# Optimization experiments

Hardware: AMD Instinct MI355X
Metric: run time of the kernel (lower is better)

The kernel has to match this reference:

```python
import jax, jax.numpy as jnp
import numpy as np

B, S, D, H = 4, 2048, 1024, 16
DK = D // H  # 64
THETA = 10000.0


def _rope(x, pos):
    # x: [..., s, d], pos: [s] int. Rotation-matrix RoPE applied to consecutive pairs.
    d = x.shape[-1]
    inv_freq = 1.0 / (THETA ** (jnp.arange(0, d, 2, dtype=jnp.float32) / d))  # [d/2]
    freqs = pos.astype(jnp.float32)[:, None] * inv_freq[None, :]             # [s, d/2]
    cos, sin = jnp.cos(freqs), jnp.sin(freqs)
    xr = x.reshape(x.shape[:-1] + (d // 2, 2))
    x0, x1 = xr[..., 0], xr[..., 1]
    y0 = cos * x0 - sin * x1
    y1 = sin * x0 + cos * x1
    return jnp.stack([y0, y1], axis=-1).reshape(x.shape)


def setup_inputs() -> dict:
    key = jax.random.key(0)
    ks = jax.random.split(key, 5)
    std = float(np.sqrt(2.0 / (D + D)))
    return {
        "x": jax.random.normal(ks[0], (B, S, D), dtype=jnp.float32),
        "token_positions": jnp.arange(S, dtype=jnp.int32),
        "wq": jax.random.normal(ks[1], (D, D), dtype=jnp.float32) * std,
        "wk": jax.random.normal(ks[2], (D, D), dtype=jnp.float32) * std,
        "wv": jax.random.normal(ks[3], (D, D), dtype=jnp.float32) * std,
        "wo": jax.random.normal(ks[4], (D, D), dtype=jnp.float32) * std,
    }


def reference(x, token_positions, wq, wk, wv, wo):
    # Linear layers use weight [out, in]: y = x @ W^T
    q = jnp.einsum('bsd,od->bso', x, wq).reshape(B, S, H, DK).transpose(0, 2, 1, 3)  # [b,h,s,dk]
    k = jnp.einsum('bsd,od->bso', x, wk).reshape(B, S, H, DK).transpose(0, 2, 1, 3)
    v = jnp.einsum('bsd,od->bso', x, wv).reshape(B, S, H, DK).transpose(0, 2, 1, 3)
    q = _rope(q, token_positions)
    k = _rope(k, token_positions)
    scores = jnp.einsum('bhqd,bhkd->bhqk', q, k) / jnp.sqrt(jnp.float32(DK))
    causal = jnp.tril(jnp.ones((S, S), dtype=bool))
    scores = jnp.where(causal, scores, jnp.finfo(scores.dtype).min)
    attn = jax.nn.softmax(scores, axis=-1)
    o = jnp.einsum('bhqk,bhkd->bhqd', attn, v)          # [b,h,s,dk]
    o = o.transpose(0, 2, 1, 3).reshape(B, S, D)        # [b,s,h*dk]
    return jnp.einsum('bsd,od->bso', o, wo)
```

## Files before the change

### kernel.cpp

```cpp
#include <hip/hip_runtime.h>
#include <hip/hip_bf16.h>
#include <stdint.h>

#define S_LEN 2048
#define NHEAD 16
#define BATCH 4

typedef __attribute__((ext_vector_type(8))) short short8;
typedef __attribute__((ext_vector_type(4))) float f32x4;
typedef __attribute__((ext_vector_type(4))) unsigned short u16x4;

__device__ float2 g_tab[131072];

__device__ __forceinline__ unsigned short f2bf(float f) {
  union { float f; uint32_t u; } a; a.f = f;
  uint32_t r = (a.u + 0x7fff + ((a.u >> 16) & 1)) >> 16;
  return (unsigned short)r;
}
__device__ __forceinline__ uint32_t pk2bf(float a, float b) {
  union { __hip_bfloat162 h; uint32_t u; } cv;
  cv.h = __float22bfloat162_rn(float2{a, b});
  return cv.u;
}

__device__ __forceinline__ void gload16(const void* g, void* l) {
  __builtin_amdgcn_global_load_lds(
      (const __attribute__((address_space(1))) void*)g,
      (__attribute__((address_space(3))) void*)l, 16, 0, 0);
}

__global__ void k_prep(const float* __restrict__ x, const float* __restrict__ wq,
                       const float* __restrict__ wk, const float* __restrict__ wv,
                       const float* __restrict__ wo, const int* __restrict__ pos,
                       unsigned short* __restrict__ xb, unsigned short* __restrict__ wdst) {
  int bid = blockIdx.x;
  if (bid < 8192) {
    int i = bid * 256 + threadIdx.x;
    float4 v = ((const float4*)x)[i];
    union { uint32_t u[2]; u16x4 v; } o;
    o.u[0] = pk2bf(v.x, v.y);
    o.u[1] = pk2bf(v.z, v.w);
    ((u16x4*)xb)[i] = o.v;
  } else if (bid < 12288) {
    int i = (bid - 8192) * 256 + threadIdx.x;
    int r = i >> 18;
    const float* s = r == 0 ? wq : r == 1 ? wk : r == 2 ? wv : wo;
    float4 v = ((const float4*)s)[i & 0x3FFFF];
    union { uint32_t u[2]; u16x4 v; } o;
    o.u[0] = pk2bf(v.x, v.y);
    o.u[1] = pk2bf(v.z, v.w);
    ((u16x4*)wdst)[i] = o.v;
  } else {
    int i = (bid - 12288) * 256 + threadIdx.x;
    int s = i >> 5, p = i & 31;
    float fp = (float)pos[s];
    float inv = exp2f(-(float)p * 0.41524101186092029f);
    float sn, cs;
    __sincosf(fp * inv, &sn, &cs);
    const float SCL = 0.18033688011112042f;
    g_tab[i] = float2{cs * SCL, sn * SCL};
    g_tab[65536 + i] = float2{cs, sn};
  }
}

template<int OUTF32, int ROPE>
__global__ __launch_bounds__(256) void k_gemm_nt(
    const unsigned short* __restrict__ A, const unsigned short* __restrict__ B,
    void* __restrict__ Cp, int K, int ldc, int gx)
{
  __shared__ unsigned short lA[128 * 64];
  __shared__ unsigned short lB[128 * 64];
  const int tid = threadIdx.x;
  const int w = tid >> 6, lane = tid & 63;
  const int wm = w >> 1, wn = w & 1;
  const int l15 = lane & 15, lg = lane >> 4;
  const int nwg = (int)gridDim.x, slot = (int)blockIdx.x;
  const int f = (slot & 7) * (nwg >> 3) + (slot >> 3);
  const int row0 = (f / gx) * 128, col0 = (f % gx) * 128;

  f32x4 acc[4][4] = {};
  const size_t rsb = (size_t)K * 2;

  for (int k0 = 0; k0 < K; k0 += 64) {
#pragma unroll
    for (int it = 0; it < 4; ++it) {
      int fb = w * 4096 + it * 1024 + lane * 16;
      int r = fb >> 7, cb = fb & 127;
      gload16((const char*)A + (size_t)(row0 + r) * rsb + k0 * 2 + cb,
              (char*)lA + (w * 4096 + it * 1024));
      gload16((const char*)B + (size_t)(col0 + r) * rsb + k0 * 2 + cb,
              (char*)lB + (w * 4096 + it * 1024));
    }
    __syncthreads();
#pragma unroll
    for (int ks = 0; ks < 2; ++ks) {
      short8 af[4], bg[4];
#pragma unroll
      for (int i = 0; i < 4; ++i) {
        int rowa = wm * 64 + i * 16 + l15;
        af[i] = *(const short8*)((const char*)lA + rowa * 128 + ks * 64 + lg * 16);
        int rowb = wn * 64 + i * 16 + l15;
        bg[i] = *(const short8*)((const char*)lB + rowb * 128 + ks * 64 + lg * 16);
      }
#pragma unroll
      for (int i = 0; i < 4; ++i)
#pragma unroll
        for (int j = 0; j < 4; ++j)
          acc[i][j] = __builtin_amdgcn_mfma_f32_16x16x32_bf16(af[i], bg[j], acc[i][j], 0, 0, 0);
    }
    __syncthreads();
  }

#pragma unroll
  for (int i = 0; i < 4; ++i)
#pragma unroll
    for (int j = 0; j < 4; ++j) {
      int col = col0 + wn * 64 + j * 16 + l15;
#pragma unroll
      for (int r = 0; r < 4; ++r) {
        int row = row0 + wm * 64 + i * 16 + lg * 4 + r;
        float v = acc[i][j][r];
        if (ROPE) {
          float vp = __shfl_xor(v, 1);
          int which = col >> 10;
          if (which < 2) {
            float2 t = g_tab[(which << 16) + ((row & (S_LEN - 1)) << 5) + ((col >> 1) & 31)];
            v = (col & 1) ? (t.y * vp + t.x * v) : (t.x * v - t.y * vp);
          }
        }
        if (OUTF32) ((float*)Cp)[(size_t)row * ldc + col] = v;
        else ((unsigned short*)Cp)[(size_t)row * ldc + col] = f2bf(v);
      }
    }
}

__global__ __launch_bounds__(512) void k_attn(const unsigned short* __restrict__ qkv,
                                              unsigned short* __restrict__ O) {
  __shared__ unsigned short lK[2][64 * 64];
  __shared__ uint32_t lV32[2][64 * 36];

  const int tid = threadIdx.x, w = tid >> 6, lane = tid & 63;
  const int l15 = lane & 15, lg = lane >> 4;
  const int slot = (int)blockIdx.x;
  const int f0 = (slot & 7) * 64 + (slot >> 3);
  const int bh = f0 >> 3, qp = f0 & 7;
  const int b = bh >> 4, h = bh & 15;
  const size_t rstride = 3072;

  short8 vr;

  auto stageK = [&](int buf, int t) {
    int fb = tid * 16;
    int r = fb >> 7;
    int cb = (fb ^ ((r & 7) << 4)) & 127;
    gload16((const char*)qkv + ((size_t)(b * S_LEN + t * 64 + r) * rstride + 1024 + h * 64) * 2 + cb,
            (char*)(&lK[buf][0]) + fb);
  };
  auto loadV = [&](int t) {
    int kp = tid >> 4, sub = tid & 15;
    int pp = sub & 1, c = (sub >> 1) * 8;
    vr = *(const short8*)(qkv + (size_t)(b * S_LEN + t * 64 + kp * 2 + pp) * rstride + 2048 + h * 64 + c);
  };
  auto writeV = [&](int buf) {
    int kp = tid >> 4, sub = tid & 15;
    int pp = sub & 1, c = (sub >> 1) * 8;
    uint32_t u0 = __shfl_xor(((const uint32_t*)&vr)[0], 1);
    uint32_t u1 = __shfl_xor(((const uint32_t*)&vr)[1], 1);
    uint32_t u2 = __shfl_xor(((const uint32_t*)&vr)[2], 1);
    uint32_t u3 = __shfl_xor(((const uint32_t*)&vr)[3], 1);
    unsigned short ov[8];
    ((uint32_t*)ov)[0] = u0; ((uint32_t*)ov)[1] = u1;
    ((uint32_t*)ov)[2] = u2; ((uint32_t*)ov)[3] = u3;
    const unsigned short* own = (const unsigned short*)&vr;
    int colk = ((kp >> 4) << 4) | (((kp >> 1) & 3) << 2) | (((kp >> 3) & 1) << 1) | (kp & 1);
#pragma unroll
    for (int j = 0; j < 4; ++j) {
      int d = c + (pp ? 4 : 0) + j;
      unsigned short lo = pp ? ov[4 + j] : own[j];
      unsigned short hi = pp ? own[4 + j] : ov[j];
      uint32_t packed = (uint32_t)lo | ((uint32_t)hi << 16);
      int colS = colk ^ (((d >> 3) & 7) << 2);
      lV32[buf][d * 36 + colS] = packed;
    }
  };

  short8 ones;
#pragma unroll
  for (int e = 0; e < 8; ++e) ones[e] = (short)0x3F80;

  for (int seg = 0; seg < 2; ++seg) {
    const int qb = (seg == 0 ? (15 - qp) : qp) * 128;
    const int ntiles = (qb >> 6) + 2;

    short8 qf[2];
    {
      int qrow = qb + w * 16 + l15;
      const unsigned short* qpt = qkv + (size_t)(b * S_LEN + qrow) * rstride + h * 64 + lg * 8;
      qf[0] = *(const short8*)qpt;
      qf[1] = *(const short8*)(qpt + 32);
    }

    float mrun = 0.f;
    f32x4 oacc[4] = {};
    f32x4 csum = {};

    stageK(0, 0);
    loadV(0);
    writeV(0);
    __syncthreads();

    for (int t = 0; t < ntiles; ++t) {
      const int cur = t & 1, nxt = cur ^ 1;
      const bool more = (t + 1 < ntiles);
      if (more) { stageK(nxt, t + 1); loadV(t + 1); }

      f32x4 sf[4] = {};
      __builtin_amdgcn_s_setprio(1);
#pragma unroll
      for (int ks = 0; ks < 2; ++ks) {
#pragma unroll
        for (int jf = 0; jf < 4; ++jf) {
          int krow = jf * 16 + l15;
          int g = krow * 128 + ks * 64 + lg * 16;
          int a = g ^ ((krow & 7) << 4);
          short8 kb = *(const short8*)((const char*)(&lK[cur][0]) + a);
          sf[jf] = __builtin_amdgcn_mfma_f32_16x16x32_bf16(kb, qf[ks], sf[jf], 0, 0, 0);
        }
      }
      __builtin_amdgcn_s_setprio(0);

      const int kv = t * 64;
      const bool dg = (kv + 63 > qb + w * 16);
      const int qglob = qb + w * 16 + l15;
      float pv[4][4];
#pragma unroll
      for (int jf = 0; jf < 4; ++jf)
#pragma unroll
        for (int r = 0; r < 4; ++r) {
          float v = sf[jf][r];
          if (dg) {
            int kglob = kv + jf * 16 + lg * 4 + r;
            if (kglob > qglob) v = -3e38f;
          }
          pv[jf][r] = v;
        }
      if (t == 0) {
        float mx = -3e38f;
#pragma unroll
        for (int jf = 0; jf < 4; ++jf)
#pragma unroll
          for (int r = 0; r < 4; ++r) mx = fmaxf(mx, pv[jf][r]);
        mx = fmaxf(mx, __shfl_xor(mx, 16));
        mx = fmaxf(mx, __shfl_xor(mx, 32));
        mrun = mx;
      }
#pragma unroll
      for (int jf = 0; jf < 4; ++jf)
#pragma unroll
        for (int r = 0; r < 4; ++r)
          pv[jf][r] = exp2f(pv[jf][r] - mrun);

      __builtin_amdgcn_s_setprio(1);
#pragma unroll
      for (int ks = 0; ks < 2; ++ks) {
        union { uint32_t u[4]; short8 v; } pb;
        pb.u[0] = pk2bf(pv[2 * ks][0], pv[2 * ks][1]);
        pb.u[1] = pk2bf(pv[2 * ks][2], pv[2 * ks][3]);
        pb.u[2] = pk2bf(pv[2 * ks + 1][0], pv[2 * ks + 1][1]);
        pb.u[3] = pk2bf(pv[2 * ks + 1][2], pv[2 * ks + 1][3]);
#pragma unroll
        for (int j = 0; j < 4; ++j) {
          int d = j * 16 + l15;
          int colS = (ks * 16 + lg * 4) ^ (((d >> 3) & 7) << 2);
          short8 vb = *(const short8*)(&lV32[cur][d * 36 + colS]);
          oacc[j] = __builtin_amdgcn_mfma_f32_16x16x32_bf16(vb, pb.v, oacc[j], 0, 0, 0);
        }
        csum = __builtin_amdgcn_mfma_f32_16x16x32_bf16(ones, pb.v, csum, 0, 0, 0);
      }
      __builtin_amdgcn_s_setprio(0);

      if (more) writeV(nxt);
      __syncthreads();

      if (!__all(csum[0] <= 1.0e9f)) {
        const float al = 0x1p-32f;
#pragma unroll
        for (int j = 0; j < 4; ++j)
#pragma unroll
          for (int r = 0; r < 4; ++r) oacc[j][r] *= al;
#pragma unroll
        for (int r = 0; r < 4; ++r) csum[r] *= al;
        mrun += 32.0f;
      }
    }

    float rinv = __builtin_amdgcn_rcpf(csum[0]);
    int qrow = qb + w * 16 + l15;
    unsigned short* orow = O + (size_t)(b * S_LEN + qrow) * 1024 + h * 64;
#pragma unroll
    for (int j = 0; j < 4; ++j) {
      union { uint32_t u[2]; u16x4 v; } ow;
      ow.u[0] = pk2bf(oacc[j][0] * rinv, oacc[j][1] * rinv);
      ow.u[1] = pk2bf(oacc[j][2] * rinv, oacc[j][3] * rinv);
      *(u16x4*)(orow + j * 16 + lg * 4) = ow.v;
    }
  }
}

extern "C" void kernel_launch(void* const* d_in, const int* in_sizes, int n_in,
                              void* d_out, int out_size, void* d_ws, size_t ws_size,
                              hipStream_t stream) {
  const float* x  = (const float*)d_in[0];
  const int* pos  = (const int*)d_in[1];
  const float* wq = (const float*)d_in[2];
  const float* wk = (const float*)d_in[3];
  const float* wv = (const float*)d_in[4];
  const float* wo = (const float*)d_in[5];
  float* out = (float*)d_out;

  char* ws = (char*)d_ws;
  unsigned short* xb   = (unsigned short*)(ws);
  unsigned short* wqkv = (unsigned short*)(ws + (size_t)16 * 1024 * 1024);
  unsigned short* wob  = (unsigned short*)(ws + (size_t)22 * 1024 * 1024);
  unsigned short* qkv  = (unsigned short*)(ws + (size_t)24 * 1024 * 1024);
  unsigned short* ob   = (unsigned short*)(ws + (size_t)72 * 1024 * 1024);

  k_prep<<<12544, 256, 0, stream>>>(x, wq, wk, wv, wo, pos, xb, wqkv);

  k_gemm_nt<0, 1><<<1536, 256, 0, stream>>>(xb, wqkv, qkv, 1024, 3072, 24);

  k_attn<<<512, 512, 0, stream>>>(qkv, ob);

  k_gemm_nt<1, 0><<<512, 256, 0, stream>>>(ob, wob, out, 1024, 1024, 8);
}
```

Measured before the change: 328.7 us.

## Double-buffer GEMM LDS tiles and move RoPE into a separate kernel

The GEMM now uses two LDS buffers per operand. The next K-tile's global-to-LDS loads are issued before the current tile's MFMAs, so load latency can overlap compute. The RoPE rotation is removed from the QKV GEMM epilogue, which dropped a shuffle and table lookup per element, and moved into a new standalone kernel that rewrites Q and K in place in bf16. The trade-offs are that LDS per block doubles to 64KB, which may reduce occupancy. The extra kernel also adds a full read and write of the Q/K part of the qkv buffer, and it applies the rotation after bf16 rounding rather than before.

```diff
diff --git a/kernel.cpp b/kernel.cpp
--- a/kernel.cpp
+++ b/kernel.cpp
@@ -16,6 +16,10 @@
   union { float f; uint32_t u; } a; a.f = f;
   uint32_t r = (a.u + 0x7fff + ((a.u >> 16) & 1)) >> 16;
   return (unsigned short)r;
+}
+__device__ __forceinline__ float bf2f(unsigned short u) {
+  union { uint32_t u; float f; } a; a.u = ((uint32_t)u) << 16;
+  return a.f;
 }
 __device__ __forceinline__ uint32_t pk2bf(float a, float b) {
   union { __hip_bfloat162 h; uint32_t u; } cv;
@@ -63,13 +67,13 @@
   }
 }
 
-template<int OUTF32, int ROPE>
+template<int OUTF32>
 __global__ __launch_bounds__(256) void k_gemm_nt(
     const unsigned short* __restrict__ A, const unsigned short* __restrict__ B,
     void* __restrict__ Cp, int K, int ldc, int gx)
 {
-  __shared__ unsigned short lA[128 * 64];
-  __shared__ unsigned short lB[128 * 64];
+  __shared__ unsigned short lA[2][128 * 64];
+  __shared__ unsigned short lB[2][128 * 64];
   const int tid = threadIdx.x;
   const int w = tid >> 6, lane = tid & 63;
   const int wm = w >> 1, wn = w & 1;
@@ -81,26 +85,35 @@
   f32x4 acc[4][4] = {};
   const size_t rsb = (size_t)K * 2;
 
-  for (int k0 = 0; k0 < K; k0 += 64) {
+  auto stage = [&](int buf, int k0) {
 #pragma unroll
     for (int it = 0; it < 4; ++it) {
       int fb = w * 4096 + it * 1024 + lane * 16;
       int r = fb >> 7, cb = fb & 127;
       gload16((const char*)A + (size_t)(row0 + r) * rsb + k0 * 2 + cb,
-              (char*)lA + (w * 4096 + it * 1024));
+              (char*)(&lA[buf][0]) + (w * 4096 + it * 1024));
       gload16((const char*)B + (size_t)(col0 + r) * rsb + k0 * 2 + cb,
-              (char*)lB + (w * 4096 + it * 1024));
-    }
-    __syncthreads();
+              (char*)(&lB[buf][0]) + (w * 4096 + it * 1024));
+    }
+  };
+
+  const int nk = K >> 6;
+  stage(0, 0);
+  __syncthreads();
+
+  for (int t = 0; t < nk; ++t) {
+    const int cur = t & 1;
+    if (t + 1 < nk) stage(cur ^ 1, (t + 1) * 64);
+
 #pragma unroll
     for (int ks = 0; ks < 2; ++ks) {
       short8 af[4], bg[4];
 #pragma unroll
       for (int i = 0; i < 4; ++i) {
         int rowa = wm * 64 + i * 16 + l15;
-        af[i] = *(const short8*)((const char*)lA + rowa * 128 + ks * 64 + lg * 16);
+        af[i] = *(const short8*)((const char*)(&lA[cur][0]) + rowa * 128 + ks * 64 + lg * 16);
         int rowb = wn * 64 + i * 16 + l15;
-        bg[i] = *(const short8*)((const char*)lB + rowb * 128 + ks * 64 + lg * 16);
+        bg[i] = *(const short8*)((const char*)(&lB[cur][0]) + rowb * 128 + ks * 64 + lg * 16);
       }
 #pragma unroll
       for (int i = 0; i < 4; ++i)
@@ -120,18 +133,34 @@
       for (int r = 0; r < 4; ++r) {
         int row = row0 + wm * 64 + i * 16 + lg * 4 + r;
         float v = acc[i][j][r];
-        if (ROPE) {
-          float vp = __shfl_xor(v, 1);
-          int which = col >> 10;
-          if (which < 2) {
-            float2 t = g_tab[(which << 16) + ((row & (S_LEN - 1)) << 5) + ((col >> 1) & 31)];
-            v = (col & 1) ? (t.y * vp + t.x * v) : (t.x * v - t.y * vp);
-          }
-        }
         if (OUTF32) ((float*)Cp)[(size_t)row * ldc + col] = v;
         else ((unsigned short*)Cp)[(size_t)row * ldc + col] = f2bf(v);
       }
     }
+}
+
+__global__ void k_rope(unsigned short* __restrict__ qkv) {
+  int idx = blockIdx.x * 256 + threadIdx.x;
+  int row = idx >> 8;
+  int rem = idx & 255;
+  int which = rem >> 7;
+  int cq = rem & 127;
+  int p0 = (cq * 4) & 31;
+  int s = row & (S_LEN - 1);
+  const float4* tb = (const float4*)&g_tab[(which << 16) + s * 32 + p0];
+  float4 t0 = tb[0], t1 = tb[1];
+  size_t off = (size_t)row * 3072 + which * 1024 + cq * 8;
+  short8 v = *(short8*)(qkv + off);
+  float x0 = bf2f((unsigned short)v[0]), x1 = bf2f((unsigned short)v[1]);
+  float x2 = bf2f((unsigned short)v[2]), x3 = bf2f((unsigned short)v[3]);
+  float x4 = bf2f((unsigned short)v[4]), x5 = bf2f((unsigned short)v[5]);
+  float x6 = bf2f((unsigned short)v[6]), x7 = bf2f((unsigned short)v[7]);
+  union { uint32_t u[4]; short8 v; } o;
+  o.u[0] = pk2bf(t0.x * x0 - t0.y * x1, t0.y * x0 + t0.x * x1);
+  o.u[1] = pk2bf(t0.z * x2 - t0.w * x3, t0.w * x2 + t0.z * x3);
+  o.u[2] = pk2bf(t1.x * x4 - t1.y * x5, t1.y * x4 + t1.x * x5);
+  o.u[3] = pk2bf(t1.z * x6 - t1.w * x7, t1.w * x6 + t1.z * x7);
+  *(short8*)(qkv + off) = o.v;
 }
 
 __global__ __launch_bounds__(512) void k_attn(const unsigned short* __restrict__ qkv,
@@ -327,9 +356,11 @@
 
   k_prep<<<12544, 256, 0, stream>>>(x, wq, wk, wv, wo, pos, xb, wqkv);
 
-  k_gemm_nt<0, 1><<<1536, 256, 0, stream>>>(xb, wqkv, qkv, 1024, 3072, 24);
+  k_gemm_nt<0><<<1536, 256, 0, stream>>>(xb, wqkv, qkv, 1024, 3072, 24);
+
+  k_rope<<<8192, 256, 0, stream>>>(qkv);
 
   k_attn<<<512, 512, 0, stream>>>(qkv, ob);
 
-  k_gemm_nt<1, 0><<<512, 256, 0, stream>>>(ob, wob, out, 1024, 1024, 8);
-}
+  k_gemm_nt<1><<<512, 256, 0, stream>>>(ob, wob, out, 1024, 1024, 8);
+}
```

Measured after the change: 284.9 us. 1.15x faster.
